# Kernel optimization log

Hardware: AMD Instinct MI355X
Metric: run time of the kernel (lower is better)

Reference implementation:

```python
import jax, jax.numpy as jnp
import numpy as np
from jax import lax

EPS = 1e-5
DN = ('NCHW', 'OIHW', 'NCHW')


def setup_inputs() -> dict:
    key = jax.random.key(0)
    ks = jax.random.split(key, 16)
    B = 8192
    # uniform(0,1): every pixel nonzero => all voxels active => sparse conv == dense conv
    x = jax.random.uniform(ks[0], (B, 1, 28, 28), dtype=jnp.float32)

    def conv_params(kw, kb, c_in, c_out, k):
        scale = 1.0 / np.sqrt(c_in * k * k)
        w = jax.random.normal(kw, (c_out, c_in, k, k), dtype=jnp.float32) * scale
        b = jax.random.normal(kb, (c_out,), dtype=jnp.float32) * scale
        return w, b

    w0, b0 = conv_params(ks[1], ks[2], 1, 32, 3)
    w1, b1 = conv_params(ks[3], ks[4], 32, 64, 2)
    w2, b2 = conv_params(ks[5], ks[6], 64, 128, 2)
    # BatchNorm affine params (init: gamma=1, beta=0)
    g0, be0 = jnp.ones((32,), jnp.float32), jnp.zeros((32,), jnp.float32)
    g1, be1 = jnp.ones((64,), jnp.float32), jnp.zeros((64,), jnp.float32)
    g2, be2 = jnp.ones((128,), jnp.float32), jnp.zeros((128,), jnp.float32)
    w_fc = jax.random.normal(ks[7], (10, 128), dtype=jnp.float32) * (1.0 / np.sqrt(128))
    b_fc = jax.random.normal(ks[8], (10,), dtype=jnp.float32) * (1.0 / np.sqrt(128))
    return dict(x=x, w0=w0, b0=b0, g0=g0, be0=be0,
                w1=w1, b1=b1, g1=g1, be1=be1,
                w2=w2, b2=b2, g2=g2, be2=be2,
                w_fc=w_fc, b_fc=b_fc)


def _conv_bn_relu(x, w, b, g, be, stride, padding):
    # sparse conv on fully-active grid == dense conv
    y = lax.conv_general_dilated(x, w, (stride, stride), padding,
                                 dimension_numbers=DN)
    y = y + b[None, :, None, None]
    # BatchNorm1d over (N_active, C) == stats over batch+spatial (biased var)
    mean = jnp.mean(y, axis=(0, 2, 3))
    var = jnp.var(y, axis=(0, 2, 3))
    y = (y - mean[None, :, None, None]) * lax.rsqrt(var + EPS)[None, :, None, None]
    y = y * g[None, :, None, None] + be[None, :, None, None]
    return jax.nn.relu(y)


def reference(x, w0, b0, g0, be0, w1, b1, g1, be1, w2, b2, g2, be2, w_fc, b_fc):
    h = _conv_bn_relu(x, w0, b0, g0, be0, 1, 'SAME')    # (B,32,28,28)
    h = _conv_bn_relu(h, w1, b1, g1, be1, 2, 'VALID')   # (B,64,14,14)
    h = _conv_bn_relu(h, w2, b2, g2, be2, 2, 'VALID')   # (B,128,7,7)
    pooled = jnp.mean(h, axis=(2, 3))                    # AdaptiveAvgPool2d(1)+Flatten
    return pooled @ w_fc.T + b_fc                        # (B, n_classes)
```

## Files before the change

kernel.cpp:

```cpp
#include <hip/hip_runtime.h>
#include <hip/hip_bf16.h>

typedef __bf16 bf16x8 __attribute__((ext_vector_type(8)));
typedef float  f32x4  __attribute__((ext_vector_type(4)));

#define BSZ 8192

union BW2 { __bf16 b[2]; unsigned int u; };
union FR  { unsigned int u[4]; bf16x8 v; };

__global__ __launch_bounds__(256) void k_stats0(const float* __restrict__ x,
                                                float* __restrict__ part0,
                                                const float* __restrict__ w1,
                                                const float* __restrict__ w2,
                                                __bf16* __restrict__ w1b,
                                                __bf16* __restrict__ w2b) {
    __shared__ float sred[4 * 54];
    const int tid = threadIdx.x;
    {
        int t = blockIdx.x * 256 + tid;
        if (t < 8192) {
            int oc = t >> 7, k = t & 127, c = k & 31, d = k >> 5;
            w1b[t] = (__bf16)w1[oc * 128 + c * 4 + d];
        }
        if (t < 32768) {
            int oc = t >> 8, k = t & 255, c = k & 63, d = k >> 6;
            w2b[t] = (__bf16)w2[oc * 256 + c * 4 + d];
        }
    }
    float a[54];
#pragma unroll
    for (int i = 0; i < 54; i++) a[i] = 0.f;
    const int total = BSZ * 784;
    for (int p = blockIdx.x * 256 + tid; p < total; p += gridDim.x * 256) {
        int b = p / 784, pix = p - b * 784;
        int y = pix / 28, xx = pix - y * 28;
        const float* xb = x + (long)b * 784;
        float nv[9];
#pragma unroll
        for (int dy = 0; dy < 3; dy++) {
            int yy = y + dy - 1;
#pragma unroll
            for (int dx = 0; dx < 3; dx++) {
                int x2 = xx + dx - 1;
                nv[dy * 3 + dx] = (yy >= 0 && yy < 28 && x2 >= 0 && x2 < 28) ? xb[yy * 28 + x2] : 0.f;
            }
        }
        int idx = 0;
#pragma unroll
        for (int t2 = 0; t2 < 9; t2++) {
            float vt = nv[t2];
            a[45 + t2] += vt;
#pragma unroll
            for (int u = t2; u < 9; u++) { a[idx] += vt * nv[u]; idx++; }
        }
    }
#pragma unroll
    for (int i = 0; i < 54; i++) {
        float v = a[i];
        v += __shfl_xor(v, 1);  v += __shfl_xor(v, 2);  v += __shfl_xor(v, 4);
        v += __shfl_xor(v, 8);  v += __shfl_xor(v, 16); v += __shfl_xor(v, 32);
        a[i] = v;
    }
    const int l = tid & 63, w = tid >> 6;
    if (l == 0) {
#pragma unroll
        for (int i = 0; i < 54; i++) sred[w * 54 + i] = a[i];
    }
    __syncthreads();
    if (tid < 54)
        part0[blockIdx.x * 64 + tid] = sred[tid] + sred[54 + tid] + sred[108 + tid] + sred[162 + tid];
}

__global__ void k_fin0(const float* __restrict__ part0, const float* __restrict__ w0,
                       const float* __restrict__ g0, const float* __restrict__ be0,
                       float* __restrict__ abc0, __bf16* __restrict__ wcv) {
    __shared__ float red[4 * 54];
    int t = threadIdx.x, c = t & 63, g = t >> 6;
    if (c < 54) {
        float acc = 0.f;
        for (int i = g; i < 1008; i += 4) acc += part0[i * 64 + c];
        red[g * 54 + c] = acc;
    }
    __syncthreads();
    if (t < 54) red[t] = red[t] + red[54 + t] + red[108 + t] + red[162 + t];
    __syncthreads();
    if (t < 32) {
        float wv[9];
#pragma unroll
        for (int tap = 0; tap < 9; tap++) wv[tap] = w0[t * 9 + tap];
        float sum = 0.f, sq = 0.f;
        int idx = 0;
#pragma unroll
        for (int ta = 0; ta < 9; ta++) {
            sum = fmaf(wv[ta], red[45 + ta], sum);
#pragma unroll
            for (int u = ta; u < 9; u++) {
                float coef = (u == ta) ? 1.f : 2.f;
                sq = fmaf(coef * wv[ta] * wv[u], red[idx], sq);
                idx++;
            }
        }
        float cnt = (float)BSZ * 784.f;
        float mean = sum / cnt;
        float var = sq / cnt - mean * mean;
        float A = g0[t] * rsqrtf(var + 1e-5f);
        abc0[288 + t] = be0[t] - mean * A;
        int nn = t >> 1, hh = t & 1;
#pragma unroll
        for (int j = 0; j < 4; j++) {
#pragma unroll
            for (int e = 0; e < 8; e++) {
                float vm = 0.f, vc = 0.f;
                if (j < 3) {
                    int i = e >> 1;
                    if (i < 3) vm = A * wv[j * 3 + i];
                    if (e < 3) {
                        float wfull = A * wv[j * 3 + e];
                        vc = wfull - (float)((__bf16)wfull);
                    }
                }
                wcv[hh * 512 + j * 128 + nn * 8 + e]       = (__bf16)vm;
                wcv[(2 + hh) * 512 + j * 128 + nn * 8 + e] = (__bf16)vc;
            }
        }
    }
}

__global__ __launch_bounds__(64, 3) void k_conv01(const float* __restrict__ x,
                                                  const float* __restrict__ abc0,
                                                  const __bf16* __restrict__ wcv,
                                                  const __bf16* __restrict__ w1b,
                                                  __bf16* __restrict__ h1,
                                                  float* __restrict__ part1) {
    __shared__ unsigned int xs2[31 * 30];
    __shared__ __attribute__((aligned(16))) __bf16 sAt[16 * 136];
    const int l = threadIdx.x;
    const int q = l >> 4, n = l & 15;
    const int b = blockIdx.x;
    for (int i = l; i < 930; i += 64) xs2[i] = 0u;
    bf16x8 bw[2][2];
#pragma unroll
    for (int ps = 0; ps < 2; ps++)
#pragma unroll
        for (int h = 0; h < 2; h++)
            bw[ps][h] = *(const bf16x8*)&wcv[(ps * 2 + h) * 512 + q * 128 + n * 8];
    const float bias0 = abc0[288 + 2 * n];
    const float bias1 = abc0[288 + 2 * n + 1];
    bf16x8 fbv[4][4];
#pragma unroll
    for (int g = 0; g < 4; g++)
#pragma unroll
        for (int kc = 0; kc < 4; kc++)
            fbv[g][kc] = *(const bf16x8*)&w1b[(g * 16 + n) * 128 + kc * 32 + q * 8];

    for (int jj = l; jj < 784; jj += 64) {
        int yy = jj / 28, xx2 = jj - yy * 28;
        float f = x[(long)b * 784 + jj];
        __bf16 hi = (__bf16)f;
        __bf16 lo = (__bf16)(f - (float)hi);
        BW2 pk; pk.b[0] = hi; pk.b[1] = lo;
        xs2[(yy + 1) * 30 + xx2 + 1] = pk.u;
    }

    float ssum[4], ssq[4];
#pragma unroll
    for (int g = 0; g < 4; g++) { ssum[g] = 0.f; ssq[g] = 0.f; }
    int my = (n >= 14) ? 1 : 0;
    int mx = n - my * 14;
    __bf16* hb = h1 + (long)b * 12544 + q * 256 + n;

    auto produce = [&](int mt, bool last) {
        int myv = my, mxv = mx;
        if (last) {
            bool pad = (n >= 4);
            myv = pad ? 13 : my;
            mxv = pad ? 13 : mx;
        }
        const int rowb = 2 * myv + q, colb = 2 * mxv;
#pragma unroll
        for (int t = 0; t < 4; t++) {
            const int d1 = t >> 1, d0 = t & 1;
            const unsigned int* p = &xs2[(rowb + d1) * 30 + colb + d0];
            unsigned int u0 = p[0], u1 = p[1], u2 = p[2];
            FR a0, a1;
            a0.u[0] = u0; a0.u[1] = u1; a0.u[2] = u2; a0.u[3] = 0u;
            a1.u[0] = (u0 & 0xffffu) | (u1 << 16); a1.u[1] = u2 & 0xffffu;
            a1.u[2] = 0u; a1.u[3] = 0u;
            f32x4 ac0 = {bias0, bias0, bias0, bias0};
            f32x4 ac1 = {bias1, bias1, bias1, bias1};
            ac0 = __builtin_amdgcn_mfma_f32_16x16x32_bf16(a0.v, bw[0][0], ac0, 0, 0, 0);
            ac1 = __builtin_amdgcn_mfma_f32_16x16x32_bf16(a0.v, bw[0][1], ac1, 0, 0, 0);
            ac0 = __builtin_amdgcn_mfma_f32_16x16x32_bf16(a1.v, bw[1][0], ac0, 0, 0, 0);
            ac1 = __builtin_amdgcn_mfma_f32_16x16x32_bf16(a1.v, bw[1][1], ac1, 0, 0, 0);
#pragma unroll
            for (int r = 0; r < 4; r++) {
                float v0 = fmaxf(ac0[r], 0.f), v1 = fmaxf(ac1[r], 0.f);
                if (last && q != 0) { v0 = 0.f; v1 = 0.f; }
                BW2 pk; pk.b[0] = (__bf16)v0; pk.b[1] = (__bf16)v1;
                *(unsigned int*)&sAt[(q * 4 + r) * 136 + t * 32 + 2 * n] = pk.u;
            }
        }
    };

    for (int mt = 0; mt < 13; mt++) {
        if (mt < 12) produce(mt, false); else produce(mt, true);
        mx += 2; my += 1;
        if (mx >= 14) { mx -= 14; my += 1; }
        bf16x8 fav[4];
        const __bf16* sa = &sAt[n * 136 + q * 8];
#pragma unroll
        for (int kc = 0; kc < 4; kc++) fav[kc] = *(const bf16x8*)&sa[kc * 32];
        const bool valid = (mt < 12) | (q == 0);
        __builtin_amdgcn_s_setprio(1);
#pragma unroll
        for (int g = 0; g < 4; g++) {
            f32x4 acc = {0.f, 0.f, 0.f, 0.f};
#pragma unroll
            for (int kc = 0; kc < 4; kc++)
                acc = __builtin_amdgcn_mfma_f32_16x16x32_bf16(fav[kc], fbv[g][kc], acc, 0, 0, 0);
#pragma unroll
            for (int r = 0; r < 4; r++) {
                if (valid) hb[mt * 1024 + r * 64 + g * 16] = (__bf16)acc[r];
                ssum[g] += acc[r]; ssq[g] += acc[r] * acc[r];
            }
        }
        __builtin_amdgcn_s_setprio(0);
    }
#pragma unroll
    for (int g = 0; g < 4; g++) {
        ssum[g] += __shfl_xor(ssum[g], 16); ssum[g] += __shfl_xor(ssum[g], 32);
        ssq[g]  += __shfl_xor(ssq[g], 16);  ssq[g]  += __shfl_xor(ssq[g], 32);
    }
    if (l < 16) {
#pragma unroll
        for (int g = 0; g < 4; g++) {
            part1[(long)(g * 16 + l) * BSZ + b] = ssum[g];
            part1[(long)(64 + g * 16 + l) * BSZ + b] = ssq[g];
        }
    }
}

__global__ __launch_bounds__(256) void k_redfin(const float* __restrict__ part,
                                                const float* __restrict__ g,
                                                const float* __restrict__ be,
                                                float* __restrict__ abc,
                                                int C, float cnt) {
    __shared__ float s1[256], s2[256];
    const int c = blockIdx.x, tid = threadIdx.x;
    float a = 0.f, bq = 0.f;
    const float* p1 = part + (long)c * BSZ;
    const float* p2 = part + (long)(C + c) * BSZ;
    for (int i = tid; i < BSZ; i += 256) { a += p1[i]; bq += p2[i]; }
    s1[tid] = a; s2[tid] = bq;
    __syncthreads();
    for (int s = 128; s > 0; s >>= 1) {
        if (tid < s) { s1[tid] += s1[tid + s]; s2[tid] += s2[tid + s]; }
        __syncthreads();
    }
    if (tid == 0) {
        float mean = s1[0] / cnt;
        float var = s2[0] / cnt - mean * mean;
        float A = g[c] * rsqrtf(var + 1e-5f);
        abc[c] = A;
        abc[C + c] = be[c] - mean * A;
    }
}

__global__ __launch_bounds__(256) void k_conv2s(__bf16* __restrict__ h1,
                                                const __bf16* __restrict__ w2b,
                                                const float* __restrict__ abc1,
                                                float* __restrict__ part2) {
    __shared__ __attribute__((aligned(16))) __bf16 sAt[2][16 * 264];
    __shared__ __attribute__((aligned(16))) __bf16 zt[16 * 136];
    __shared__ float sbn1[128];
    const int tid = threadIdx.x;
    if (tid < 128) sbn1[tid] = abc1[tid];
    const int w = tid >> 6, l = tid & 63, q = l >> 4, n = l & 15;
    bf16x8 fbv[2][8];
#pragma unroll
    for (int ntl = 0; ntl < 2; ntl++) {
        int oc = w * 32 + 2 * n + ntl;
#pragma unroll
        for (int kc = 0; kc < 8; kc++)
            fbv[ntl][kc] = *(const bf16x8*)&w2b[oc * 256 + kc * 32 + q * 8];
    }
    __syncthreads();

    for (int img = 0; img < 4; img++) {
        const int b = blockIdx.x * 4 + img;
        __bf16* src = h1 + (long)b * 12544;
        float ssum[2] = {0.f, 0.f}, ssq[2] = {0.f, 0.f};
        for (int mt = 0; mt < 4; mt++) {
#pragma unroll
            for (int it = 0; it < 2; it++) {
                int idx = it * 256 + tid;
                int rl = idx >> 5, o = (idx & 31) * 8;
                int r = mt * 16 + rl;
                bf16x8 wv;
                if (r < 49) {
                    int d = o >> 6, c = o & 63;
                    int py = r / 7, px = r - py * 7;
                    int msrc = (2 * py + (d >> 1)) * 14 + 2 * px + (d & 1);
                    bf16x8 v = *(const bf16x8*)&src[msrc * 64 + c];
#pragma unroll
                    for (int j = 0; j < 8; j++) {
                        float f = fmaxf((float)v[j] * sbn1[c + j] + sbn1[64 + c + j], 0.f);
                        wv[j] = (__bf16)f;
                    }
                } else {
#pragma unroll
                    for (int j = 0; j < 8; j++) wv[j] = (__bf16)0.0f;
                }
                *(bf16x8*)&sAt[mt & 1][rl * 264 + o] = wv;
            }
            __syncthreads();
            bf16x8 fav[8];
#pragma unroll
            for (int kc = 0; kc < 8; kc++)
                fav[kc] = *(const bf16x8*)&sAt[mt & 1][n * 264 + kc * 32 + q * 8];
            f32x4 accA = {0.f, 0.f, 0.f, 0.f}, accB = {0.f, 0.f, 0.f, 0.f};
#pragma unroll
            for (int kc = 0; kc < 8; kc++) {
                accA = __builtin_amdgcn_mfma_f32_16x16x32_bf16(fav[kc], fbv[0][kc], accA, 0, 0, 0);
                accB = __builtin_amdgcn_mfma_f32_16x16x32_bf16(fav[kc], fbv[1][kc], accB, 0, 0, 0);
            }
#pragma unroll
            for (int rr = 0; rr < 4; rr++) {
                BW2 pk; pk.b[0] = (__bf16)accA[rr]; pk.b[1] = (__bf16)accB[rr];
                *(unsigned int*)&zt[(q * 4 + rr) * 136 + w * 32 + 2 * n] = pk.u;
                ssum[0] += accA[rr]; ssq[0] += accA[rr] * accA[rr];
                ssum[1] += accB[rr]; ssq[1] += accB[rr] * accB[rr];
            }
            __syncthreads();
            {
                int row = tid >> 4, o = (tid & 15) * 8;
                int m = mt * 16 + row;
                if (m < 49) {
                    bf16x8 zv = *(const bf16x8*)&zt[row * 136 + o];
                    *(bf16x8*)&src[m * 128 + o] = zv;
                }
            }
        }
#pragma unroll
        for (int ntl = 0; ntl < 2; ntl++) {
            ssum[ntl] += __shfl_xor(ssum[ntl], 16); ssum[ntl] += __shfl_xor(ssum[ntl], 32);
            ssq[ntl]  += __shfl_xor(ssq[ntl], 16);  ssq[ntl]  += __shfl_xor(ssq[ntl], 32);
        }
        if (l < 16) {
#pragma unroll
            for (int ntl = 0; ntl < 2; ntl++) {
                int oc = w * 32 + 2 * l + ntl;
                part2[(long)oc * BSZ + b] = ssum[ntl];
                part2[(long)(128 + oc) * BSZ + b] = ssq[ntl];
            }
        }
    }
}

__global__ __launch_bounds__(256) void k_final(const __bf16* __restrict__ z2,
                                               const float* __restrict__ abc2,
                                               const float* __restrict__ wfc,
                                               const float* __restrict__ bfc,
                                               float* __restrict__ out) {
    __shared__ float sbn2[256];
    __shared__ float pp[16 * 128];
    __shared__ float pooled[128];
    __shared__ float fcred[80];
    const int tid = threadIdx.x;
    sbn2[tid] = abc2[tid];
    __syncthreads();
    const int g = tid & 15, c0 = g * 8, rg = tid >> 4;
    for (int img = 0; img < 4; img++) {
        const int b = blockIdx.x * 4 + img;
        const __bf16* src = z2 + (long)b * 12544;
        float acc[8];
#pragma unroll
        for (int q = 0; q < 8; q++) acc[q] = 0.f;
        for (int rr = rg; rr < 49; rr += 16) {
            bf16x8 v = *(const bf16x8*)&src[rr * 128 + c0];
#pragma unroll
            for (int q = 0; q < 8; q++) {
                float f = fmaxf((float)v[q] * sbn2[c0 + q] + sbn2[128 + c0 + q], 0.f);
                acc[q] += f;
            }
        }
        *(f32x4*)&pp[rg * 128 + c0]     = *(f32x4*)&acc[0];
        *(f32x4*)&pp[rg * 128 + c0 + 4] = *(f32x4*)&acc[4];
        __syncthreads();
        if (tid < 128) {
            float s = 0.f;
#pragma unroll
            for (int r = 0; r < 16; r++) s += pp[r * 128 + tid];
            pooled[tid] = s * (1.f / 49.f);
        }
        __syncthreads();
        if (tid < 80) {
            int o = tid >> 3, s = tid & 7;
            float a = 0.f;
#pragma unroll
            for (int j = 0; j < 16; j++) a = fmaf(pooled[s * 16 + j], wfc[o * 128 + s * 16 + j], a);
            fcred[tid] = a;
        }
        __syncthreads();
        if (tid < 10) {
            float a = bfc[tid];
#pragma unroll
            for (int s = 0; s < 8; s++) a += fcred[tid * 8 + s];
            out[(long)b * 10 + tid] = a;
        }
    }
}

extern "C" void kernel_launch(void* const* d_in, const int* in_sizes, int n_in,
                              void* d_out, int out_size, void* d_ws, size_t ws_size,
                              hipStream_t stream) {
    const float* x   = (const float*)d_in[0];
    const float* w0  = (const float*)d_in[1];
    const float* g0  = (const float*)d_in[3];
    const float* be0 = (const float*)d_in[4];
    const float* w1  = (const float*)d_in[5];
    const float* g1  = (const float*)d_in[7];
    const float* be1 = (const float*)d_in[8];
    const float* w2  = (const float*)d_in[9];
    const float* g2  = (const float*)d_in[11];
    const float* be2 = (const float*)d_in[12];
    const float* wfc = (const float*)d_in[13];
    const float* bfc = (const float*)d_in[14];
    float* out = (float*)d_out;

    float* ws    = (float*)d_ws;
    float* part0 = ws;
    __bf16* wcv  = (__bf16*)(part0 + 1008 * 64);
    float* abc0  = part0 + 1024 * 64;
    float* part1 = abc0 + 320;
    float* abc1  = part1 + 128 * BSZ;
    float* part2 = abc1 + 128;
    float* abc2  = part2 + 256 * BSZ;
    __bf16* w1b  = (__bf16*)(abc2 + 256);
    __bf16* w2b  = w1b + 8192;
    __bf16* h1   = w2b + 32768;

    k_stats0<<<dim3(1008), dim3(256), 0, stream>>>(x, part0, w1, w2, w1b, w2b);
    k_fin0<<<dim3(1), dim3(256), 0, stream>>>(part0, w0, g0, be0, abc0, wcv);
    k_conv01<<<dim3(BSZ), dim3(64), 0, stream>>>(x, abc0, wcv, w1b, h1, part1);
    k_redfin<<<dim3(64), dim3(256), 0, stream>>>(part1, g1, be1, abc1, 64, (float)(BSZ * 196));
    k_conv2s<<<dim3(BSZ / 4), dim3(256), 0, stream>>>(h1, w2b, abc1, part2);
    k_redfin<<<dim3(128), dim3(256), 0, stream>>>(part2, g2, be2, abc2, 128, (float)(BSZ * 49));
    k_final<<<dim3(BSZ / 4), dim3(256), 0, stream>>>(h1, abc2, wfc, bfc, out);
}
```

Baseline: 388.3 us.

## Recompute conv0/conv1 per pass instead of storing h1 to global memory

Drops the global h1 intermediate. Conv0+conv1 are recomputed from x in each of three passes: stats only, then conv2 stats, then conv2 plus pool plus FC. Conv0 is repacked into a single MFMA pair per tap, with the bias folded into the K dimension as hi/lo bf16 constants. This removes large global writes and reads of the bf16 activations at the cost of redoing the conv0/conv1 MFMA work three times. Conv1 output channel order is remapped, and layer-2 output goes straight into pooling with no z2 writeback.

```diff
diff --git a/kernel.cpp b/kernel.cpp
--- a/kernel.cpp
+++ b/kernel.cpp
@@ -74,7 +74,7 @@
 
 __global__ void k_fin0(const float* __restrict__ part0, const float* __restrict__ w0,
                        const float* __restrict__ g0, const float* __restrict__ be0,
-                       float* __restrict__ abc0, __bf16* __restrict__ wcv) {
+                       __bf16* __restrict__ wcv) {
     __shared__ float red[4 * 54];
     int t = threadIdx.x, c = t & 63, g = t >> 6;
     if (c < 54) {
@@ -105,124 +105,133 @@
         float mean = sum / cnt;
         float var = sq / cnt - mean * mean;
         float A = g0[t] * rsqrtf(var + 1e-5f);
-        abc0[288 + t] = be0[t] - mean * A;
+        float bias = be0[t] - mean * A;
+        __bf16 bhi = (__bf16)bias;
+        float blo = bias - (float)bhi;
         int nn = t >> 1, hh = t & 1;
 #pragma unroll
-        for (int j = 0; j < 4; j++) {
+        for (int qq = 0; qq < 4; qq++) {
 #pragma unroll
             for (int e = 0; e < 8; e++) {
-                float vm = 0.f, vc = 0.f;
-                if (j < 3) {
-                    int i = e >> 1;
-                    if (i < 3) vm = A * wv[j * 3 + i];
-                    if (e < 3) {
-                        float wfull = A * wv[j * 3 + e];
-                        vc = wfull - (float)((__bf16)wfull);
+                float v = 0.f;
+                if (qq < 3) {
+                    if (e < 6) {
+                        int i = e >> 1;
+                        v = (float)((__bf16)(A * wv[qq * 3 + i]));
+                    } else if (e == 6) {
+                        float wf = A * wv[qq * 3 + 0]; v = wf - (float)((__bf16)wf);
+                    } else {
+                        float wf = A * wv[qq * 3 + 1]; v = wf - (float)((__bf16)wf);
                     }
+                } else {
+                    if (e == 0)      { float wf = A * wv[2]; v = wf - (float)((__bf16)wf); }
+                    else if (e == 1) { float wf = A * wv[5]; v = wf - (float)((__bf16)wf); }
+                    else if (e == 2) { float wf = A * wv[8]; v = wf - (float)((__bf16)wf); }
+                    else if (e == 4) v = (float)bhi;
+                    else if (e == 5) v = blo;
                 }
-                wcv[hh * 512 + j * 128 + nn * 8 + e]       = (__bf16)vm;
-                wcv[(2 + hh) * 512 + j * 128 + nn * 8 + e] = (__bf16)vc;
-            }
-        }
-    }
-}
-
-__global__ __launch_bounds__(64, 3) void k_conv01(const float* __restrict__ x,
-                                                  const float* __restrict__ abc0,
-                                                  const __bf16* __restrict__ wcv,
-                                                  const __bf16* __restrict__ w1b,
-                                                  __bf16* __restrict__ h1,
-                                                  float* __restrict__ part1) {
-    __shared__ unsigned int xs2[31 * 30];
-    __shared__ __attribute__((aligned(16))) __bf16 sAt[16 * 136];
-    const int l = threadIdx.x;
-    const int q = l >> 4, n = l & 15;
-    const int b = blockIdx.x;
-    for (int i = l; i < 930; i += 64) xs2[i] = 0u;
-    bf16x8 bw[2][2];
-#pragma unroll
-    for (int ps = 0; ps < 2; ps++)
-#pragma unroll
-        for (int h = 0; h < 2; h++)
-            bw[ps][h] = *(const bf16x8*)&wcv[(ps * 2 + h) * 512 + q * 128 + n * 8];
-    const float bias0 = abc0[288 + 2 * n];
-    const float bias1 = abc0[288 + 2 * n + 1];
-    bf16x8 fbv[4][4];
-#pragma unroll
-    for (int g = 0; g < 4; g++)
-#pragma unroll
-        for (int kc = 0; kc < 4; kc++)
-            fbv[g][kc] = *(const bf16x8*)&w1b[(g * 16 + n) * 128 + kc * 32 + q * 8];
-
-    for (int jj = l; jj < 784; jj += 64) {
+                wcv[hh * 512 + qq * 128 + nn * 8 + e] = (__bf16)v;
+            }
+        }
+    }
+}
+
+struct C0S {
+    bf16x8 bwM0, bwM1;
+    int q, n;
+    int Koff, off1, off2;
+    bool q3;
+};
+
+__device__ inline void c0_init(C0S& S, const __bf16* __restrict__ wcv, int l) {
+    S.q = l >> 4; S.n = l & 15; S.q3 = (S.q == 3);
+    S.bwM0 = *(const bf16x8*)&wcv[S.q * 128 + S.n * 8];
+    S.bwM1 = *(const bf16x8*)&wcv[512 + S.q * 128 + S.n * 8];
+    S.Koff = S.q3 ? 2 : S.q * 30;
+    S.off1 = S.q3 ? 30 : 1;
+    S.off2 = S.q3 ? 60 : 2;
+}
+
+__device__ inline void c0_produce(const C0S& S, const unsigned* __restrict__ xs2w,
+                                  __bf16* sAtw, int my, int mx, bool zpad) {
+    const int b00 = 2 * my * 30 + 2 * mx + S.Koff;
+#pragma unroll
+    for (int t = 0; t < 4; t++) {
+        const int d1 = t >> 1, d0 = t & 1;
+        const unsigned* p = xs2w + b00 + d1 * 30 + d0;
+        unsigned v0 = p[0], v1 = p[S.off1], v2 = p[S.off2];
+        unsigned pm = __builtin_amdgcn_perm(v1, v0, 0x05040100u);
+        FR A;
+        A.u[0] = S.q3 ? pm : v0;
+        A.u[1] = S.q3 ? (v2 & 0xffffu) : v1;
+        A.u[2] = S.q3 ? 0x3F803F80u : v2;
+        A.u[3] = S.q3 ? 0u : pm;
+        f32x4 z = {0.f, 0.f, 0.f, 0.f};
+        f32x4 ac0 = __builtin_amdgcn_mfma_f32_16x16x32_bf16(A.v, S.bwM0, z, 0, 0, 0);
+        f32x4 ac1 = __builtin_amdgcn_mfma_f32_16x16x32_bf16(A.v, S.bwM1, z, 0, 0, 0);
+#pragma unroll
+        for (int r = 0; r < 4; r++) {
+            float a0 = fmaxf(ac0[r], 0.f), a1 = fmaxf(ac1[r], 0.f);
+            if (zpad) { a0 = 0.f; a1 = 0.f; }
+            BW2 pk; pk.b[0] = (__bf16)a0; pk.b[1] = (__bf16)a1;
+            *(unsigned*)&sAtw[(S.q * 4 + r) * 136 + t * 32 + 2 * S.n] = pk.u;
+        }
+    }
+}
+
+__device__ inline void stage_img(unsigned* xs2w, const float* __restrict__ x,
+                                 long b, int t0, int stride) {
+    for (int jj = t0; jj < 784; jj += stride) {
         int yy = jj / 28, xx2 = jj - yy * 28;
-        float f = x[(long)b * 784 + jj];
+        float f = x[b * 784 + jj];
         __bf16 hi = (__bf16)f;
         __bf16 lo = (__bf16)(f - (float)hi);
         BW2 pk; pk.b[0] = hi; pk.b[1] = lo;
-        xs2[(yy + 1) * 30 + xx2 + 1] = pk.u;
-    }
-
-    float ssum[4], ssq[4];
-#pragma unroll
-    for (int g = 0; g < 4; g++) { ssum[g] = 0.f; ssq[g] = 0.f; }
-    int my = (n >= 14) ? 1 : 0;
-    int mx = n - my * 14;
-    __bf16* hb = h1 + (long)b * 12544 + q * 256 + n;
-
-    auto produce = [&](int mt, bool last) {
-        int myv = my, mxv = mx;
-        if (last) {
-            bool pad = (n >= 4);
-            myv = pad ? 13 : my;
-            mxv = pad ? 13 : mx;
-        }
-        const int rowb = 2 * myv + q, colb = 2 * mxv;
-#pragma unroll
-        for (int t = 0; t < 4; t++) {
-            const int d1 = t >> 1, d0 = t & 1;
-            const unsigned int* p = &xs2[(rowb + d1) * 30 + colb + d0];
-            unsigned int u0 = p[0], u1 = p[1], u2 = p[2];
-            FR a0, a1;
-            a0.u[0] = u0; a0.u[1] = u1; a0.u[2] = u2; a0.u[3] = 0u;
-            a1.u[0] = (u0 & 0xffffu) | (u1 << 16); a1.u[1] = u2 & 0xffffu;
-            a1.u[2] = 0u; a1.u[3] = 0u;
-            f32x4 ac0 = {bias0, bias0, bias0, bias0};
-            f32x4 ac1 = {bias1, bias1, bias1, bias1};
-            ac0 = __builtin_amdgcn_mfma_f32_16x16x32_bf16(a0.v, bw[0][0], ac0, 0, 0, 0);
-            ac1 = __builtin_amdgcn_mfma_f32_16x16x32_bf16(a0.v, bw[0][1], ac1, 0, 0, 0);
-            ac0 = __builtin_amdgcn_mfma_f32_16x16x32_bf16(a1.v, bw[1][0], ac0, 0, 0, 0);
-            ac1 = __builtin_amdgcn_mfma_f32_16x16x32_bf16(a1.v, bw[1][1], ac1, 0, 0, 0);
+        xs2w[(yy + 1) * 30 + xx2 + 1] = pk.u;
+    }
+}
+
+__global__ __launch_bounds__(256, 4) void k_convA(const float* __restrict__ x,
+                                                  const __bf16* __restrict__ wcv,
+                                                  const __bf16* __restrict__ w1b,
+                                                  float* __restrict__ part1) {
+    __shared__ unsigned xs2a[4][900];
+    __shared__ __attribute__((aligned(16))) __bf16 sAta[4][16 * 136];
+    const int tid = threadIdx.x, w = tid >> 6, l = tid & 63;
+    const int q = l >> 4, n = l & 15;
+    unsigned* xs2w = xs2a[w];
+    __bf16* sAtw = sAta[w];
+    C0S S0; c0_init(S0, wcv, l);
+    bf16x8 fbv[4][4];
+#pragma unroll
+    for (int g = 0; g < 4; g++)
+#pragma unroll
+        for (int kc = 0; kc < 4; kc++)
+            fbv[g][kc] = *(const bf16x8*)&w1b[(4 * n + g) * 128 + kc * 32 + q * 8];
+    const long b = (long)blockIdx.x * 4 + w;
+    for (int i = l; i < 900; i += 64) xs2w[i] = 0u;
+    stage_img(xs2w, x, b, l, 64);
+    float ssum[4] = {0.f, 0.f, 0.f, 0.f}, ssq[4] = {0.f, 0.f, 0.f, 0.f};
+    for (int mt = 0; mt < 13; mt++) {
+        const bool last = (mt == 12);
+        int mv = (last && n >= 4) ? 195 : mt * 16 + n;
+        int my = mv / 14, mx = mv - my * 14;
+        c0_produce(S0, xs2w, sAtw, my, mx, last && (q != 0));
+        const __bf16* sa = &sAtw[n * 136 + q * 8];
+        bf16x8 fav[4];
+#pragma unroll
+        for (int kc = 0; kc < 4; kc++) fav[kc] = *(const bf16x8*)&sa[kc * 32];
+        __builtin_amdgcn_s_setprio(1);
+#pragma unroll
+        for (int g = 0; g < 4; g++) {
+            f32x4 a = {0.f, 0.f, 0.f, 0.f};
+#pragma unroll
+            for (int kc = 0; kc < 4; kc++)
+                a = __builtin_amdgcn_mfma_f32_16x16x32_bf16(fav[kc], fbv[g][kc], a, 0, 0, 0);
 #pragma unroll
             for (int r = 0; r < 4; r++) {
-                float v0 = fmaxf(ac0[r], 0.f), v1 = fmaxf(ac1[r], 0.f);
-                if (last && q != 0) { v0 = 0.f; v1 = 0.f; }
-                BW2 pk; pk.b[0] = (__bf16)v0; pk.b[1] = (__bf16)v1;
-                *(unsigned int*)&sAt[(q * 4 + r) * 136 + t * 32 + 2 * n] = pk.u;
-            }
-        }
-    };
-
-    for (int mt = 0; mt < 13; mt++) {
-        if (mt < 12) produce(mt, false); else produce(mt, true);
-        mx += 2; my += 1;
-        if (mx >= 14) { mx -= 14; my += 1; }
-        bf16x8 fav[4];
-        const __bf16* sa = &sAt[n * 136 + q * 8];
-#pragma unroll
-        for (int kc = 0; kc < 4; kc++) fav[kc] = *(const bf16x8*)&sa[kc * 32];
-        const bool valid = (mt < 12) | (q == 0);
-        __builtin_amdgcn_s_setprio(1);
-#pragma unroll
-        for (int g = 0; g < 4; g++) {
-            f32x4 acc = {0.f, 0.f, 0.f, 0.f};
-#pragma unroll
-            for (int kc = 0; kc < 4; kc++)
-                acc = __builtin_amdgcn_mfma_f32_16x16x32_bf16(fav[kc], fbv[g][kc], acc, 0, 0, 0);
-#pragma unroll
-            for (int r = 0; r < 4; r++) {
-                if (valid) hb[mt * 1024 + r * 64 + g * 16] = (__bf16)acc[r];
-                ssum[g] += acc[r]; ssq[g] += acc[r] * acc[r];
+                ssum[g] += a[r];
+                ssq[g] = fmaf(a[r], a[r], ssq[g]);
             }
         }
         __builtin_amdgcn_s_setprio(0);
@@ -235,8 +244,8 @@
     if (l < 16) {
 #pragma unroll
         for (int g = 0; g < 4; g++) {
-            part1[(long)(g * 16 + l) * BSZ + b] = ssum[g];
-            part1[(long)(64 + g * 16 + l) * BSZ + b] = ssq[g];
+            part1[(long)(4 * l + g) * BSZ + b] = ssum[g];
+            part1[(long)(64 + 4 * l + g) * BSZ + b] = ssq[g];
         }
     }
 }
@@ -267,31 +276,74 @@
     }
 }
 
-__global__ __launch_bounds__(256) void k_conv2s(__bf16* __restrict__ h1,
-                                                const __bf16* __restrict__ w2b,
-                                                const float* __restrict__ abc1,
-                                                float* __restrict__ part2) {
-    __shared__ __attribute__((aligned(16))) __bf16 sAt[2][16 * 264];
-    __shared__ __attribute__((aligned(16))) __bf16 zt[16 * 136];
+__global__ __launch_bounds__(256, 3) void k_convB(const float* __restrict__ x,
+                                                  const __bf16* __restrict__ wcv,
+                                                  const __bf16* __restrict__ w1b,
+                                                  const __bf16* __restrict__ w2b,
+                                                  const float* __restrict__ abc1,
+                                                  float* __restrict__ part2) {
+    __shared__ __attribute__((aligned(16))) unsigned char U[21008];
+    __shared__ __attribute__((aligned(16))) __bf16 h1L[196 * 64];
     __shared__ float sbn1[128];
-    const int tid = threadIdx.x;
+    const int tid = threadIdx.x, w = tid >> 6, l = tid & 63;
+    const int q = l >> 4, n = l & 15;
+    unsigned* xs2w = (unsigned*)(U + 17408);
+    __bf16* sAtw = (__bf16*)(U + w * 4352);
+    __bf16* sAt2 = (__bf16*)U;
+    C0S S0; c0_init(S0, wcv, l);
     if (tid < 128) sbn1[tid] = abc1[tid];
-    const int w = tid >> 6, l = tid & 63, q = l >> 4, n = l & 15;
-    bf16x8 fbv[2][8];
-#pragma unroll
-    for (int ntl = 0; ntl < 2; ntl++) {
-        int oc = w * 32 + 2 * n + ntl;
-#pragma unroll
-        for (int kc = 0; kc < 8; kc++)
-            fbv[ntl][kc] = *(const bf16x8*)&w2b[oc * 256 + kc * 32 + q * 8];
-    }
+    for (int i = tid; i < 900; i += 256) xs2w[i] = 0u;
     __syncthreads();
 
     for (int img = 0; img < 4; img++) {
-        const int b = blockIdx.x * 4 + img;
-        __bf16* src = h1 + (long)b * 12544;
-        float ssum[2] = {0.f, 0.f}, ssq[2] = {0.f, 0.f};
+        const long b = (long)blockIdx.x * 4 + img;
+        stage_img(xs2w, x, b, tid, 256);
+        __syncthreads();
+        {
+            bf16x8 fbv[4][4];
+#pragma unroll
+            for (int g = 0; g < 4; g++)
+#pragma unroll
+                for (int kc = 0; kc < 4; kc++)
+                    fbv[g][kc] = *(const bf16x8*)&w1b[(4 * n + g) * 128 + kc * 32 + q * 8];
+            for (int mt = w; mt < 13; mt += 4) {
+                const bool last = (mt == 12);
+                int mv = (last && n >= 4) ? 195 : mt * 16 + n;
+                int my = mv / 14, mx = mv - my * 14;
+                c0_produce(S0, xs2w, sAtw, my, mx, last && (q != 0));
+                const __bf16* sa = &sAtw[n * 136 + q * 8];
+                bf16x8 fav[4];
+#pragma unroll
+                for (int kc = 0; kc < 4; kc++) fav[kc] = *(const bf16x8*)&sa[kc * 32];
+                const bool valid = (mt < 12) | (q == 0);
+                __builtin_amdgcn_s_setprio(1);
+#pragma unroll
+                for (int g = 0; g < 4; g++) {
+                    f32x4 a = {0.f, 0.f, 0.f, 0.f};
+#pragma unroll
+                    for (int kc = 0; kc < 4; kc++)
+                        a = __builtin_amdgcn_mfma_f32_16x16x32_bf16(fav[kc], fbv[g][kc], a, 0, 0, 0);
+                    if (valid) {
+#pragma unroll
+                        for (int r = 0; r < 4; r++)
+                            h1L[(mt * 16 + q * 4 + r) * 64 + 4 * n + g] = (__bf16)a[r];
+                    }
+                }
+                __builtin_amdgcn_s_setprio(0);
+            }
+        }
+        __syncthreads();
+        bf16x8 fbv2[2][8];
+#pragma unroll
+        for (int ntl = 0; ntl < 2; ntl++) {
+            int oc = (2 * w + ntl) * 16 + n;
+#pragma unroll
+            for (int kc = 0; kc < 8; kc++)
+                fbv2[ntl][kc] = *(const bf16x8*)&w2b[oc * 256 + kc * 32 + q * 8];
+        }
+        float s2a = 0.f, s2b = 0.f, q2a = 0.f, q2b = 0.f;
         for (int mt = 0; mt < 4; mt++) {
+            __bf16* sb = sAt2 + (mt & 1) * 4224;
 #pragma unroll
             for (int it = 0; it < 2; it++) {
                 int idx = it * 256 + tid;
@@ -302,104 +354,175 @@
                     int d = o >> 6, c = o & 63;
                     int py = r / 7, px = r - py * 7;
                     int msrc = (2 * py + (d >> 1)) * 14 + 2 * px + (d & 1);
-                    bf16x8 v = *(const bf16x8*)&src[msrc * 64 + c];
-#pragma unroll
-                    for (int j = 0; j < 8; j++) {
-                        float f = fmaxf((float)v[j] * sbn1[c + j] + sbn1[64 + c + j], 0.f);
-                        wv[j] = (__bf16)f;
-                    }
+                    bf16x8 v = *(const bf16x8*)&h1L[msrc * 64 + c];
+#pragma unroll
+                    for (int j = 0; j < 8; j++)
+                        wv[j] = (__bf16)fmaxf((float)v[j] * sbn1[c + j] + sbn1[64 + c + j], 0.f);
                 } else {
 #pragma unroll
                     for (int j = 0; j < 8; j++) wv[j] = (__bf16)0.0f;
                 }
-                *(bf16x8*)&sAt[mt & 1][rl * 264 + o] = wv;
+                *(bf16x8*)&sb[rl * 264 + o] = wv;
             }
             __syncthreads();
             bf16x8 fav[8];
 #pragma unroll
             for (int kc = 0; kc < 8; kc++)
-                fav[kc] = *(const bf16x8*)&sAt[mt & 1][n * 264 + kc * 32 + q * 8];
-            f32x4 accA = {0.f, 0.f, 0.f, 0.f}, accB = {0.f, 0.f, 0.f, 0.f};
+                fav[kc] = *(const bf16x8*)&sb[n * 264 + kc * 32 + q * 8];
+            f32x4 aA = {0.f, 0.f, 0.f, 0.f}, aB = {0.f, 0.f, 0.f, 0.f};
 #pragma unroll
             for (int kc = 0; kc < 8; kc++) {
-                accA = __builtin_amdgcn_mfma_f32_16x16x32_bf16(fav[kc], fbv[0][kc], accA, 0, 0, 0);
-                accB = __builtin_amdgcn_mfma_f32_16x16x32_bf16(fav[kc], fbv[1][kc], accB, 0, 0, 0);
+                aA = __builtin_amdgcn_mfma_f32_16x16x32_bf16(fav[kc], fbv2[0][kc], aA, 0, 0, 0);
+                aB = __builtin_amdgcn_mfma_f32_16x16x32_bf16(fav[kc], fbv2[1][kc], aB, 0, 0, 0);
             }
 #pragma unroll
             for (int rr = 0; rr < 4; rr++) {
-                BW2 pk; pk.b[0] = (__bf16)accA[rr]; pk.b[1] = (__bf16)accB[rr];
-                *(unsigned int*)&zt[(q * 4 + rr) * 136 + w * 32 + 2 * n] = pk.u;
-                ssum[0] += accA[rr]; ssq[0] += accA[rr] * accA[rr];
-                ssum[1] += accB[rr]; ssq[1] += accB[rr] * accB[rr];
+                s2a += aA[rr]; q2a = fmaf(aA[rr], aA[rr], q2a);
+                s2b += aB[rr]; q2b = fmaf(aB[rr], aB[rr], q2b);
+            }
+        }
+        s2a += __shfl_xor(s2a, 16); s2a += __shfl_xor(s2a, 32);
+        q2a += __shfl_xor(q2a, 16); q2a += __shfl_xor(q2a, 32);
+        s2b += __shfl_xor(s2b, 16); s2b += __shfl_xor(s2b, 32);
+        q2b += __shfl_xor(q2b, 16); q2b += __shfl_xor(q2b, 32);
+        if (l < 16) {
+            int oc0 = (2 * w + 0) * 16 + l, oc1 = (2 * w + 1) * 16 + l;
+            part2[(long)oc0 * BSZ + b] = s2a;
+            part2[(long)(128 + oc0) * BSZ + b] = q2a;
+            part2[(long)oc1 * BSZ + b] = s2b;
+            part2[(long)(128 + oc1) * BSZ + b] = q2b;
+        }
+    }
+}
+
+__global__ __launch_bounds__(256, 3) void k_convC(const float* __restrict__ x,
+                                                  const __bf16* __restrict__ wcv,
+                                                  const __bf16* __restrict__ w1b,
+                                                  const __bf16* __restrict__ w2b,
+                                                  const float* __restrict__ abc1,
+                                                  const float* __restrict__ abc2,
+                                                  const float* __restrict__ wfc,
+                                                  const float* __restrict__ bfc,
+                                                  float* __restrict__ out) {
+    __shared__ __attribute__((aligned(16))) unsigned char U[21008];
+    __shared__ __attribute__((aligned(16))) __bf16 h1L[196 * 64];
+    __shared__ float sbn1[128];
+    __shared__ float pooledL[128];
+    __shared__ float fcred[80];
+    const int tid = threadIdx.x, w = tid >> 6, l = tid & 63;
+    const int q = l >> 4, n = l & 15;
+    unsigned* xs2w = (unsigned*)(U + 17408);
+    __bf16* sAtw = (__bf16*)(U + w * 4352);
+    __bf16* sAt2 = (__bf16*)U;
+    C0S S0; c0_init(S0, wcv, l);
+    if (tid < 128) sbn1[tid] = abc1[tid];
+    const float a20 = abc2[(2 * w + 0) * 16 + n], b20 = abc2[128 + (2 * w + 0) * 16 + n];
+    const float a21 = abc2[(2 * w + 1) * 16 + n], b21 = abc2[128 + (2 * w + 1) * 16 + n];
+    for (int i = tid; i < 900; i += 256) xs2w[i] = 0u;
+    __syncthreads();
+
+    for (int img = 0; img < 4; img++) {
+        const long b = (long)blockIdx.x * 4 + img;
+        stage_img(xs2w, x, b, tid, 256);
+        __syncthreads();
+        {
+            bf16x8 fbv[4][4];
+#pragma unroll
+            for (int g = 0; g < 4; g++)
+#pragma unroll
+                for (int kc = 0; kc < 4; kc++)
+                    fbv[g][kc] = *(const bf16x8*)&w1b[(4 * n + g) * 128 + kc * 32 + q * 8];
+            for (int mt = w; mt < 13; mt += 4) {
+                const bool last = (mt == 12);
+                int mv = (last && n >= 4) ? 195 : mt * 16 + n;
+                int my = mv / 14, mx = mv - my * 14;
+                c0_produce(S0, xs2w, sAtw, my, mx, last && (q != 0));
+                const __bf16* sa = &sAtw[n * 136 + q * 8];
+                bf16x8 fav[4];
+#pragma unroll
+                for (int kc = 0; kc < 4; kc++) fav[kc] = *(const bf16x8*)&sa[kc * 32];
+                const bool valid = (mt < 12) | (q == 0);
+                __builtin_amdgcn_s_setprio(1);
+#pragma unroll
+                for (int g = 0; g < 4; g++) {
+                    f32x4 a = {0.f, 0.f, 0.f, 0.f};
+#pragma unroll
+                    for (int kc = 0; kc < 4; kc++)
+                        a = __builtin_amdgcn_mfma_f32_16x16x32_bf16(fav[kc], fbv[g][kc], a, 0, 0, 0);
+                    if (valid) {
+#pragma unroll
+                        for (int r = 0; r < 4; r++)
+                            h1L[(mt * 16 + q * 4 + r) * 64 + 4 * n + g] = (__bf16)a[r];
+                    }
+                }
+                __builtin_amdgcn_s_setprio(0);
+            }
+        }
+        __syncthreads();
+        bf16x8 fbv2[2][8];
+#pragma unroll
+        for (int ntl = 0; ntl < 2; ntl++) {
+            int oc = (2 * w + ntl) * 16 + n;
+#pragma unroll
+            for (int kc = 0; kc < 8; kc++)
+                fbv2[ntl][kc] = *(const bf16x8*)&w2b[oc * 256 + kc * 32 + q * 8];
+        }
+        float pl0 = 0.f, pl1 = 0.f;
+        for (int mt = 0; mt < 4; mt++) {
+            __bf16* sb = sAt2 + (mt & 1) * 4224;
+#pragma unroll
+            for (int it = 0; it < 2; it++) {
+                int idx = it * 256 + tid;
+                int rl = idx >> 5, o = (idx & 31) * 8;
+                int r = mt * 16 + rl;
+                bf16x8 wv;
+                if (r < 49) {
+                    int d = o >> 6, c = o & 63;
+                    int py = r / 7, px = r - py * 7;
+                    int msrc = (2 * py + (d >> 1)) * 14 + 2 * px + (d & 1);
+                    bf16x8 v = *(const bf16x8*)&h1L[msrc * 64 + c];
+#pragma unroll
+                    for (int j = 0; j < 8; j++)
+                        wv[j] = (__bf16)fmaxf((float)v[j] * sbn1[c + j] + sbn1[64 + c + j], 0.f);
+                } else {
+#pragma unroll
+                    for (int j = 0; j < 8; j++) wv[j] = (__bf16)0.0f;
+                }
+                *(bf16x8*)&sb[rl * 264 + o] = wv;
             }
             __syncthreads();
-            {
-                int row = tid >> 4, o = (tid & 15) * 8;
-                int m = mt * 16 + row;
-                if (m < 49) {
-                    bf16x8 zv = *(const bf16x8*)&zt[row * 136 + o];
-                    *(bf16x8*)&src[m * 128 + o] = zv;
+            bf16x8 fav[8];
+#pragma unroll
+            for (int kc = 0; kc < 8; kc++)
+                fav[kc] = *(const bf16x8*)&sb[n * 264 + kc * 32 + q * 8];
+            f32x4 aA = {0.f, 0.f, 0.f, 0.f}, aB = {0.f, 0.f, 0.f, 0.f};
+#pragma unroll
+            for (int kc = 0; kc < 8; kc++) {
+                aA = __builtin_amdgcn_mfma_f32_16x16x32_bf16(fav[kc], fbv2[0][kc], aA, 0, 0, 0);
+                aB = __builtin_amdgcn_mfma_f32_16x16x32_bf16(fav[kc], fbv2[1][kc], aB, 0, 0, 0);
+            }
+#pragma unroll
+            for (int rr = 0; rr < 4; rr++) {
+                int pos = mt * 16 + q * 4 + rr;
+                if (pos < 49) {
+                    pl0 += fmaxf((float)(__bf16)aA[rr] * a20 + b20, 0.f);
+                    pl1 += fmaxf((float)(__bf16)aB[rr] * a21 + b21, 0.f);
                 }
             }
         }
-#pragma unroll
-        for (int ntl = 0; ntl < 2; ntl++) {
-            ssum[ntl] += __shfl_xor(ssum[ntl], 16); ssum[ntl] += __shfl_xor(ssum[ntl], 32);
-            ssq[ntl]  += __shfl_xor(ssq[ntl], 16);  ssq[ntl]  += __shfl_xor(ssq[ntl], 32);
-        }
+        pl0 += __shfl_xor(pl0, 16); pl0 += __shfl_xor(pl0, 32);
+        pl1 += __shfl_xor(pl1, 16); pl1 += __shfl_xor(pl1, 32);
         if (l < 16) {
-#pragma unroll
-            for (int ntl = 0; ntl < 2; ntl++) {
-                int oc = w * 32 + 2 * l + ntl;
-                part2[(long)oc * BSZ + b] = ssum[ntl];
-                part2[(long)(128 + oc) * BSZ + b] = ssq[ntl];
-            }
-        }
-    }
-}
-
-__global__ __launch_bounds__(256) void k_final(const __bf16* __restrict__ z2,
-                                               const float* __restrict__ abc2,
-                                               const float* __restrict__ wfc,
-                                               const float* __restrict__ bfc,
-                                               float* __restrict__ out) {
-    __shared__ float sbn2[256];
-    __shared__ float pp[16 * 128];
-    __shared__ float pooled[128];
-    __shared__ float fcred[80];
-    const int tid = threadIdx.x;
-    sbn2[tid] = abc2[tid];
-    __syncthreads();
-    const int g = tid & 15, c0 = g * 8, rg = tid >> 4;
-    for (int img = 0; img < 4; img++) {
-        const int b = blockIdx.x * 4 + img;
-        const __bf16* src = z2 + (long)b * 12544;
-        float acc[8];
-#pragma unroll
-        for (int q = 0; q < 8; q++) acc[q] = 0.f;
-        for (int rr = rg; rr < 49; rr += 16) {
-            bf16x8 v = *(const bf16x8*)&src[rr * 128 + c0];
-#pragma unroll
-            for (int q = 0; q < 8; q++) {
-                float f = fmaxf((float)v[q] * sbn2[c0 + q] + sbn2[128 + c0 + q], 0.f);
-                acc[q] += f;
-            }
-        }
-        *(f32x4*)&pp[rg * 128 + c0]     = *(f32x4*)&acc[0];
-        *(f32x4*)&pp[rg * 128 + c0 + 4] = *(f32x4*)&acc[4];
-        __syncthreads();
-        if (tid < 128) {
-            float s = 0.f;
-#pragma unroll
-            for (int r = 0; r < 16; r++) s += pp[r * 128 + tid];
-            pooled[tid] = s * (1.f / 49.f);
+            pooledL[(2 * w + 0) * 16 + l] = pl0 * (1.f / 49.f);
+            pooledL[(2 * w + 1) * 16 + l] = pl1 * (1.f / 49.f);
         }
         __syncthreads();
         if (tid < 80) {
             int o = tid >> 3, s = tid & 7;
             float a = 0.f;
 #pragma unroll
-            for (int j = 0; j < 16; j++) a = fmaf(pooled[s * 16 + j], wfc[o * 128 + s * 16 + j], a);
+            for (int j = 0; j < 16; j++)
+                a = fmaf(pooledL[s * 16 + j], wfc[o * 128 + s * 16 + j], a);
             fcred[tid] = a;
         }
         __syncthreads();
@@ -407,7 +530,7 @@
             float a = bfc[tid];
 #pragma unroll
             for (int s = 0; s < 8; s++) a += fcred[tid * 8 + s];
-            out[(long)b * 10 + tid] = a;
+            out[b * 10 + tid] = a;
         }
     }
 }
@@ -439,13 +562,12 @@
     float* abc2  = part2 + 256 * BSZ;
     __bf16* w1b  = (__bf16*)(abc2 + 256);
     __bf16* w2b  = w1b + 8192;
-    __bf16* h1   = w2b + 32768;
 
     k_stats0<<<dim3(1008), dim3(256), 0, stream>>>(x, part0, w1, w2, w1b, w2b);
-    k_fin0<<<dim3(1), dim3(256), 0, stream>>>(part0, w0, g0, be0, abc0, wcv);
-    k_conv01<<<dim3(BSZ), dim3(64), 0, stream>>>(x, abc0, wcv, w1b, h1, part1);
+    k_fin0<<<dim3(1), dim3(256), 0, stream>>>(part0, w0, g0, be0, wcv);
+    k_convA<<<dim3(BSZ / 4), dim3(256), 0, stream>>>(x, wcv, w1b, part1);
     k_redfin<<<dim3(64), dim3(256), 0, stream>>>(part1, g1, be1, abc1, 64, (float)(BSZ * 196));
-    k_conv2s<<<dim3(BSZ / 4), dim3(256), 0, stream>>>(h1, w2b, abc1, part2);
+    k_convB<<<dim3(BSZ / 4), dim3(256), 0, stream>>>(x, wcv, w1b, w2b, abc1, part2);
     k_redfin<<<dim3(128), dim3(256), 0, stream>>>(part2, g2, be2, abc2, 128, (float)(BSZ * 49));
-    k_final<<<dim3(BSZ / 4), dim3(256), 0, stream>>>(h1, abc2, wfc, bfc, out);
-}
+    k_convC<<<dim3(BSZ / 4), dim3(256), 0, stream>>>(x, wcv, w1b, w2b, abc1, abc2, wfc, bfc, out);
+}
```

Result: slower. 748.3 us (+92.7%).

## Fold conv0 bias and split-precision terms into one MFMA pair; batch 4 images per block

Applied to the files above, without the earlier changes.

Conv0 weights are repacked so that the hi/lo split terms and the BN bias (as a bf16 hi/lo pair multiplied by a constant 1.0 lane) share a single K=32 MFMA. This halves the conv0 MFMAs per tile from four to two and drops the bias loads. k_conv01 now runs four images per 256-thread block, one wave each with private LDS, instead of one 64-thread block per image. The conv1 weight channel order is permuted so each lane writes four contiguous bf16 outputs as a single 8-byte store, with the partial-stat indexing changed to match. The risks are subtle precision and indexing changes and higher LDS use per block.

```diff
diff --git a/kernel.cpp b/kernel.cpp
--- a/kernel.cpp
+++ b/kernel.cpp
@@ -74,7 +74,7 @@
 
 __global__ void k_fin0(const float* __restrict__ part0, const float* __restrict__ w0,
                        const float* __restrict__ g0, const float* __restrict__ be0,
-                       float* __restrict__ abc0, __bf16* __restrict__ wcv) {
+                       __bf16* __restrict__ wcv) {
     __shared__ float red[4 * 54];
     int t = threadIdx.x, c = t & 63, g = t >> 6;
     if (c < 54) {
@@ -105,113 +105,125 @@
         float mean = sum / cnt;
         float var = sq / cnt - mean * mean;
         float A = g0[t] * rsqrtf(var + 1e-5f);
-        abc0[288 + t] = be0[t] - mean * A;
+        float bias = be0[t] - mean * A;
+        __bf16 bhi = (__bf16)bias;
+        float blo = bias - (float)bhi;
         int nn = t >> 1, hh = t & 1;
 #pragma unroll
-        for (int j = 0; j < 4; j++) {
+        for (int qq = 0; qq < 4; qq++) {
 #pragma unroll
             for (int e = 0; e < 8; e++) {
-                float vm = 0.f, vc = 0.f;
-                if (j < 3) {
-                    int i = e >> 1;
-                    if (i < 3) vm = A * wv[j * 3 + i];
-                    if (e < 3) {
-                        float wfull = A * wv[j * 3 + e];
-                        vc = wfull - (float)((__bf16)wfull);
+                float v = 0.f;
+                if (qq < 3) {
+                    if (e < 6) {
+                        int i = e >> 1;
+                        v = (float)((__bf16)(A * wv[qq * 3 + i]));
+                    } else if (e == 6) {
+                        float wf = A * wv[qq * 3 + 0]; v = wf - (float)((__bf16)wf);
+                    } else {
+                        float wf = A * wv[qq * 3 + 1]; v = wf - (float)((__bf16)wf);
                     }
+                } else {
+                    if (e == 0)      { float wf = A * wv[2]; v = wf - (float)((__bf16)wf); }
+                    else if (e == 1) { float wf = A * wv[5]; v = wf - (float)((__bf16)wf); }
+                    else if (e == 2) { float wf = A * wv[8]; v = wf - (float)((__bf16)wf); }
+                    else if (e == 4) v = (float)bhi;
+                    else if (e == 5) v = blo;
                 }
-                wcv[hh * 512 + j * 128 + nn * 8 + e]       = (__bf16)vm;
-                wcv[(2 + hh) * 512 + j * 128 + nn * 8 + e] = (__bf16)vc;
-            }
-        }
-    }
-}
-
-__global__ __launch_bounds__(64, 3) void k_conv01(const float* __restrict__ x,
-                                                  const float* __restrict__ abc0,
-                                                  const __bf16* __restrict__ wcv,
-                                                  const __bf16* __restrict__ w1b,
-                                                  __bf16* __restrict__ h1,
-                                                  float* __restrict__ part1) {
-    __shared__ unsigned int xs2[31 * 30];
-    __shared__ __attribute__((aligned(16))) __bf16 sAt[16 * 136];
-    const int l = threadIdx.x;
-    const int q = l >> 4, n = l & 15;
-    const int b = blockIdx.x;
-    for (int i = l; i < 930; i += 64) xs2[i] = 0u;
-    bf16x8 bw[2][2];
-#pragma unroll
-    for (int ps = 0; ps < 2; ps++)
-#pragma unroll
-        for (int h = 0; h < 2; h++)
-            bw[ps][h] = *(const bf16x8*)&wcv[(ps * 2 + h) * 512 + q * 128 + n * 8];
-    const float bias0 = abc0[288 + 2 * n];
-    const float bias1 = abc0[288 + 2 * n + 1];
-    bf16x8 fbv[4][4];
-#pragma unroll
-    for (int g = 0; g < 4; g++)
-#pragma unroll
-        for (int kc = 0; kc < 4; kc++)
-            fbv[g][kc] = *(const bf16x8*)&w1b[(g * 16 + n) * 128 + kc * 32 + q * 8];
-
-    for (int jj = l; jj < 784; jj += 64) {
+                wcv[hh * 512 + qq * 128 + nn * 8 + e] = (__bf16)v;
+            }
+        }
+    }
+}
+
+struct C0S {
+    bf16x8 bwM0, bwM1;
+    int q, n;
+    int Koff, off1, off2;
+    bool q3;
+};
+
+__device__ inline void c0_init(C0S& S, const __bf16* __restrict__ wcv, int l) {
+    S.q = l >> 4; S.n = l & 15; S.q3 = (S.q == 3);
+    S.bwM0 = *(const bf16x8*)&wcv[S.q * 128 + S.n * 8];
+    S.bwM1 = *(const bf16x8*)&wcv[512 + S.q * 128 + S.n * 8];
+    S.Koff = S.q3 ? 2 : S.q * 30;
+    S.off1 = S.q3 ? 30 : 1;
+    S.off2 = S.q3 ? 60 : 2;
+}
+
+__device__ inline void c0_produce(const C0S& S, const unsigned* __restrict__ xs2w,
+                                  __bf16* sAtw, int my, int mx, bool zpad) {
+    const int b00 = 2 * my * 30 + 2 * mx + S.Koff;
+#pragma unroll
+    for (int t = 0; t < 4; t++) {
+        const int d1 = t >> 1, d0 = t & 1;
+        const unsigned* p = xs2w + b00 + d1 * 30 + d0;
+        unsigned v0 = p[0], v1 = p[S.off1], v2 = p[S.off2];
+        unsigned pm = __builtin_amdgcn_perm(v1, v0, 0x05040100u);
+        FR A;
+        A.u[0] = S.q3 ? pm : v0;
+        A.u[1] = S.q3 ? (v2 & 0xffffu) : v1;
+        A.u[2] = S.q3 ? 0x3F803F80u : v2;
+        A.u[3] = S.q3 ? 0u : pm;
+        f32x4 z = {0.f, 0.f, 0.f, 0.f};
+        f32x4 ac0 = __builtin_amdgcn_mfma_f32_16x16x32_bf16(A.v, S.bwM0, z, 0, 0, 0);
+        f32x4 ac1 = __builtin_amdgcn_mfma_f32_16x16x32_bf16(A.v, S.bwM1, z, 0, 0, 0);
+#pragma unroll
+        for (int r = 0; r < 4; r++) {
+            float a0 = fmaxf(ac0[r], 0.f), a1 = fmaxf(ac1[r], 0.f);
+            if (zpad) { a0 = 0.f; a1 = 0.f; }
+            BW2 pk; pk.b[0] = (__bf16)a0; pk.b[1] = (__bf16)a1;
+            *(unsigned*)&sAtw[(S.q * 4 + r) * 136 + t * 32 + 2 * S.n] = pk.u;
+        }
+    }
+}
+
+__device__ inline void stage_img(unsigned* xs2w, const float* __restrict__ x,
+                                 long b, int t0, int stride) {
+    for (int jj = t0; jj < 784; jj += stride) {
         int yy = jj / 28, xx2 = jj - yy * 28;
-        float f = x[(long)b * 784 + jj];
+        float f = x[b * 784 + jj];
         __bf16 hi = (__bf16)f;
         __bf16 lo = (__bf16)(f - (float)hi);
         BW2 pk; pk.b[0] = hi; pk.b[1] = lo;
-        xs2[(yy + 1) * 30 + xx2 + 1] = pk.u;
-    }
-
-    float ssum[4], ssq[4];
-#pragma unroll
-    for (int g = 0; g < 4; g++) { ssum[g] = 0.f; ssq[g] = 0.f; }
-    int my = (n >= 14) ? 1 : 0;
-    int mx = n - my * 14;
-    __bf16* hb = h1 + (long)b * 12544 + q * 256 + n;
-
-    auto produce = [&](int mt, bool last) {
-        int myv = my, mxv = mx;
-        if (last) {
-            bool pad = (n >= 4);
-            myv = pad ? 13 : my;
-            mxv = pad ? 13 : mx;
-        }
-        const int rowb = 2 * myv + q, colb = 2 * mxv;
-#pragma unroll
-        for (int t = 0; t < 4; t++) {
-            const int d1 = t >> 1, d0 = t & 1;
-            const unsigned int* p = &xs2[(rowb + d1) * 30 + colb + d0];
-            unsigned int u0 = p[0], u1 = p[1], u2 = p[2];
-            FR a0, a1;
-            a0.u[0] = u0; a0.u[1] = u1; a0.u[2] = u2; a0.u[3] = 0u;
-            a1.u[0] = (u0 & 0xffffu) | (u1 << 16); a1.u[1] = u2 & 0xffffu;
-            a1.u[2] = 0u; a1.u[3] = 0u;
-            f32x4 ac0 = {bias0, bias0, bias0, bias0};
-            f32x4 ac1 = {bias1, bias1, bias1, bias1};
-            ac0 = __builtin_amdgcn_mfma_f32_16x16x32_bf16(a0.v, bw[0][0], ac0, 0, 0, 0);
-            ac1 = __builtin_amdgcn_mfma_f32_16x16x32_bf16(a0.v, bw[0][1], ac1, 0, 0, 0);
-            ac0 = __builtin_amdgcn_mfma_f32_16x16x32_bf16(a1.v, bw[1][0], ac0, 0, 0, 0);
-            ac1 = __builtin_amdgcn_mfma_f32_16x16x32_bf16(a1.v, bw[1][1], ac1, 0, 0, 0);
-#pragma unroll
-            for (int r = 0; r < 4; r++) {
-                float v0 = fmaxf(ac0[r], 0.f), v1 = fmaxf(ac1[r], 0.f);
-                if (last && q != 0) { v0 = 0.f; v1 = 0.f; }
-                BW2 pk; pk.b[0] = (__bf16)v0; pk.b[1] = (__bf16)v1;
-                *(unsigned int*)&sAt[(q * 4 + r) * 136 + t * 32 + 2 * n] = pk.u;
-            }
-        }
-    };
-
+        xs2w[(yy + 1) * 30 + xx2 + 1] = pk.u;
+    }
+}
+
+__global__ __launch_bounds__(256, 4) void k_conv01(const float* __restrict__ x,
+                                                   const __bf16* __restrict__ wcv,
+                                                   const __bf16* __restrict__ w1b,
+                                                   __bf16* __restrict__ h1,
+                                                   float* __restrict__ part1) {
+    __shared__ unsigned xs2a[4][900];
+    __shared__ __attribute__((aligned(16))) __bf16 sAta[4][16 * 136];
+    const int tid = threadIdx.x, w = tid >> 6, l = tid & 63;
+    const int q = l >> 4, n = l & 15;
+    unsigned* xs2w = xs2a[w];
+    __bf16* sAtw = sAta[w];
+    C0S S0; c0_init(S0, wcv, l);
+    bf16x8 fbv[4][4];
+#pragma unroll
+    for (int g = 0; g < 4; g++)
+#pragma unroll
+        for (int kc = 0; kc < 4; kc++)
+            fbv[g][kc] = *(const bf16x8*)&w1b[(4 * n + g) * 128 + kc * 32 + q * 8];
+    const long b = (long)blockIdx.x * 4 + w;
+    for (int i = l; i < 900; i += 64) xs2w[i] = 0u;
+    stage_img(xs2w, x, b, l, 64);
+    float ssum[4] = {0.f, 0.f, 0.f, 0.f}, ssq[4] = {0.f, 0.f, 0.f, 0.f};
+    __bf16* hb = h1 + b * 12544;
     for (int mt = 0; mt < 13; mt++) {
-        if (mt < 12) produce(mt, false); else produce(mt, true);
-        mx += 2; my += 1;
-        if (mx >= 14) { mx -= 14; my += 1; }
+        const bool last = (mt == 12);
+        int mv = (last && n >= 4) ? 195 : mt * 16 + n;
+        int my = mv / 14, mx = mv - my * 14;
+        c0_produce(S0, xs2w, sAtw, my, mx, last && (q != 0));
+        const __bf16* sa = &sAtw[n * 136 + q * 8];
         bf16x8 fav[4];
-        const __bf16* sa = &sAt[n * 136 + q * 8];
 #pragma unroll
         for (int kc = 0; kc < 4; kc++) fav[kc] = *(const bf16x8*)&sa[kc * 32];
-        const bool valid = (mt < 12) | (q == 0);
+        f32x4 a[4];
         __builtin_amdgcn_s_setprio(1);
 #pragma unroll
         for (int g = 0; g < 4; g++) {
@@ -219,13 +231,26 @@
 #pragma unroll
             for (int kc = 0; kc < 4; kc++)
                 acc = __builtin_amdgcn_mfma_f32_16x16x32_bf16(fav[kc], fbv[g][kc], acc, 0, 0, 0);
+            a[g] = acc;
+        }
+        __builtin_amdgcn_s_setprio(0);
+#pragma unroll
+        for (int g = 0; g < 4; g++)
 #pragma unroll
             for (int r = 0; r < 4; r++) {
-                if (valid) hb[mt * 1024 + r * 64 + g * 16] = (__bf16)acc[r];
-                ssum[g] += acc[r]; ssq[g] += acc[r] * acc[r];
-            }
-        }
-        __builtin_amdgcn_s_setprio(0);
+                ssum[g] += a[g][r];
+                ssq[g] = fmaf(a[g][r], a[g][r], ssq[g]);
+            }
+        if ((mt < 12) | (q == 0)) {
+#pragma unroll
+            for (int r = 0; r < 4; r++) {
+                BW2 p0, p1;
+                p0.b[0] = (__bf16)a[0][r]; p0.b[1] = (__bf16)a[1][r];
+                p1.b[0] = (__bf16)a[2][r]; p1.b[1] = (__bf16)a[3][r];
+                uint2 u; u.x = p0.u; u.y = p1.u;
+                *(uint2*)&hb[(mt * 16 + q * 4 + r) * 64 + 4 * n] = u;
+            }
+        }
     }
 #pragma unroll
     for (int g = 0; g < 4; g++) {
@@ -235,8 +260,8 @@
     if (l < 16) {
 #pragma unroll
         for (int g = 0; g < 4; g++) {
-            part1[(long)(g * 16 + l) * BSZ + b] = ssum[g];
-            part1[(long)(64 + g * 16 + l) * BSZ + b] = ssq[g];
+            part1[(long)(4 * l + g) * BSZ + b] = ssum[g];
+            part1[(long)(64 + 4 * l + g) * BSZ + b] = ssq[g];
         }
     }
 }
@@ -329,8 +354,8 @@
             for (int rr = 0; rr < 4; rr++) {
                 BW2 pk; pk.b[0] = (__bf16)accA[rr]; pk.b[1] = (__bf16)accB[rr];
                 *(unsigned int*)&zt[(q * 4 + rr) * 136 + w * 32 + 2 * n] = pk.u;
-                ssum[0] += accA[rr]; ssq[0] += accA[rr] * accA[rr];
-                ssum[1] += accB[rr]; ssq[1] += accB[rr] * accB[rr];
+                ssum[0] += accA[rr]; ssq[0] = fmaf(accA[rr], accA[rr], ssq[0]);
+                ssum[1] += accB[rr]; ssq[1] = fmaf(accB[rr], accB[rr], ssq[1]);
             }
             __syncthreads();
             {
@@ -442,8 +467,8 @@
     __bf16* h1   = w2b + 32768;
 
     k_stats0<<<dim3(1008), dim3(256), 0, stream>>>(x, part0, w1, w2, w1b, w2b);
-    k_fin0<<<dim3(1), dim3(256), 0, stream>>>(part0, w0, g0, be0, abc0, wcv);
-    k_conv01<<<dim3(BSZ), dim3(64), 0, stream>>>(x, abc0, wcv, w1b, h1, part1);
+    k_fin0<<<dim3(1), dim3(256), 0, stream>>>(part0, w0, g0, be0, wcv);
+    k_conv01<<<dim3(BSZ / 4), dim3(256), 0, stream>>>(x, wcv, w1b, h1, part1);
     k_redfin<<<dim3(64), dim3(256), 0, stream>>>(part1, g1, be1, abc1, 64, (float)(BSZ * 196));
     k_conv2s<<<dim3(BSZ / 4), dim3(256), 0, stream>>>(h1, w2b, abc1, part2);
     k_redfin<<<dim3(128), dim3(256), 0, stream>>>(part2, g2, be2, abc2, 128, (float)(BSZ * 49));
```

New measurement: 368.5 us. -5.1%, faster.
